# Kernel optimization log

Measured on AMD Instinct MI355X. Metric: run time of the kernel, lower is better.

The kernel has to match this reference:

```python
import jax, jax.numpy as jnp
import numpy as np

EMBED_DIM = 128


def setup_inputs() -> dict:
    key = jax.random.key(0)
    k = jax.random.split(key, 6)
    B, S, H, D = 4, 512, 768, EMBED_DIM
    ent_embeddings = jax.random.normal(k[0], (B, S, H), jnp.float32)
    ent_type_ids = jax.random.randint(k[1], (B, S), 0, 10)  # entity-type labels (>=0)
    ent_mask = jax.random.randint(k[2], (B, S), 0, 2)       # 0/1 attention mask
    W_mu = jax.random.normal(k[3], (H, D), jnp.float32) / np.sqrt(H)
    b_mu = jnp.zeros((D,), jnp.float32)
    W_sigma = jax.random.normal(k[4], (H, D), jnp.float32) / np.sqrt(H)
    b_sigma = jnp.zeros((D,), jnp.float32)
    return dict(ent_embeddings=ent_embeddings, ent_type_ids=ent_type_ids, ent_mask=ent_mask,
                W_mu=W_mu, b_mu=b_mu, W_sigma=W_sigma, b_sigma=b_sigma)


def _pairwise_kl(mu, sigma, dim):
    # Symmetrized KL between diagonal Gaussians for all pairs (i=row, j=col).
    # Decomposed into rank-D contractions instead of materializing [N,N,D].
    inv = 1.0 / sigma                               # [N,D]
    S_log = jnp.sum(jnp.log(sigma), axis=1)         # [N] sum_d log sigma (1e-14 inside log is negligible in fp32)
    A = jnp.einsum('id,jd->ij', inv, sigma)         # sum_d sigma_j/sigma_i
    q = jnp.sum(mu * mu * inv, axis=1)              # [N] sum_d mu_i^2/sigma_i
    cross = jnp.einsum('id,jd->ij', mu * inv, mu)   # sum_d mu_i*mu_j/sigma_i
    quad = jnp.einsum('id,jd->ij', inv, mu * mu)    # sum_d mu_j^2/sigma_i
    md_i = q[:, None] - 2.0 * cross + quad          # sum_d (mu_i-mu_j)^2 / sigma_i
    ld = S_log[None, :] - S_log[:, None]            # sum_d log(sigma_j/sigma_i)
    ij_kl = 0.5 * (A + md_i - dim - ld)
    ji_kl = 0.5 * (A.T + md_i.T - dim + ld)
    return 0.5 * (ij_kl + ji_kl)


def reference(ent_embeddings, ent_type_ids, ent_mask, W_mu, b_mu, W_sigma, b_sigma):
    D = EMBED_DIM
    h = jax.nn.relu(ent_embeddings)                 # dropout in eval mode (identity)
    mu = (h @ W_mu + b_mu).reshape(-1, D)           # [N,D]
    sigma = (jax.nn.elu(h @ W_sigma + b_sigma) + 1.0 + 1e-14).reshape(-1, D)

    labels = ent_type_ids.reshape(-1)
    valid = (ent_mask.reshape(-1) == 1) & (labels >= 0)   # consider_mutual_O=True: no labels>0 filter

    # loss_mask: ALL coordinates of mu differ (kills diagonal / duplicate rows)
    alldiff = jnp.all(mu[:, None, :] != mu[None, :, :], axis=-1)  # [N,N]
    pair_valid = valid[:, None] & valid[None, :]
    lab_eq = labels[:, None] == labels[None, :]
    denom_m = (alldiff & pair_valid).astype(mu.dtype)             # loss_mask
    num_w = (lab_eq & alldiff & pair_valid).astype(mu.dtype)      # loss_weights

    loss = -_pairwise_kl(mu, sigma, D)              # loss_type='KL'

    # NT-Xent, temperature=1
    e = jnp.exp(loss)
    cnts = jnp.sum(num_w, axis=1)
    loss_num = jnp.sum(e * num_w, axis=1)
    loss_den = jnp.sum(e * denom_m, axis=1)
    sel = cnts > 0
    safe = lambda v: jnp.where(sel, v, 1.0)
    lf = -jnp.log2(safe(loss_num)) + jnp.log2(safe(loss_den)) + jnp.log2(safe(cnts))
    n_sel = jnp.maximum(jnp.sum(sel.astype(mu.dtype)), 1.0)
    return jnp.sum(jnp.where(sel, lf, 0.0)) / n_sel
```

## Files before the change

kernel.cpp:

```cpp
#include <hip/hip_runtime.h>
#include <math.h>

#define NROWS 2048
#define HDIM 768
#define DDIM 128
#define FEAT 512
#define DCAP 2048
#define TSLOTS 8192

typedef __attribute__((ext_vector_type(8))) short bf16x8;
typedef __attribute__((ext_vector_type(4))) float f32x4;

__device__ __forceinline__ void mergeState(float& m, float& n, float& d,
                                           float m2, float n2, float d2) {
  float M = fmaxf(m, m2);
  float s1 = (m >= M) ? 1.0f : __expf(m - M);
  float s2 = (m2 >= M) ? 1.0f : __expf(m2 - M);
  n = n * s1 + n2 * s2;
  d = d * s1 + d2 * s2;
  m = M;
}

__device__ __forceinline__ unsigned short bfhi(float x) {
  unsigned int u = __float_as_uint(x);
  return (unsigned short)((u + 0x7fffu + ((u >> 16) & 1u)) >> 16);
}

__global__ __launch_bounds__(256) void k1m(
    const float* __restrict__ E, const float* __restrict__ Wmu,
    const float* __restrict__ Wsg, float* __restrict__ Cpart,
    unsigned long long* __restrict__ tab, int* __restrict__ rowflag,
    int* __restrict__ dupcnt, float* __restrict__ gsum)
{
  __shared__ unsigned short lds[12288];
  const int t = threadIdx.x;
  const int bid = blockIdx.x;

  if (t < 32) tab[bid * 32 + t] = 0ULL;
  if (t < 8)  rowflag[bid * 8 + t] = 0;
  if (bid == 0 && t == 0) {
    dupcnt[0] = 0;
    gsum[0] = 0.f; gsum[1] = 0.f; gsum[2] = 0.f;
  }

  const int mt = bid & 31, nt = (bid >> 5) & 1, ks = bid >> 6;
  const int i0 = mt * 64, kbase = ks * 192;
  const float* Wsrc = nt ? Wsg : Wmu;

  const int akg = t & 3, arow = t >> 2;
  const int bcol = t & 127, bkh = t >> 7;
  const int aw  = akg * 512 + arow * 8;
  const int bw0 = 2048 + (bkh * 2) * 1024 + bcol * 8;
  const int bw1 = bw0 + 1024;

  float4 rA0, rA1; float rB[16];

  auto loadRegs = [&](int it) {
    const int ka = kbase + it * 32;
    const float* ep = E + (size_t)(i0 + arow) * HDIM + ka + akg * 8;
    rA0 = *reinterpret_cast<const float4*>(ep);
    rA1 = *reinterpret_cast<const float4*>(ep + 4);
    const float* wp = Wsrc + (size_t)(ka + bkh * 16) * DDIM + bcol;
    #pragma unroll
    for (int j = 0; j < 16; ++j) rB[j] = wp[(size_t)j * DDIM];
  };

  auto writeLds = [&](int buf) {
    unsigned short* lb = lds + buf * 6144;
    unsigned short ha[8];
    ha[0] = bfhi(fmaxf(rA0.x, 0.f)); ha[1] = bfhi(fmaxf(rA0.y, 0.f));
    ha[2] = bfhi(fmaxf(rA0.z, 0.f)); ha[3] = bfhi(fmaxf(rA0.w, 0.f));
    ha[4] = bfhi(fmaxf(rA1.x, 0.f)); ha[5] = bfhi(fmaxf(rA1.y, 0.f));
    ha[6] = bfhi(fmaxf(rA1.z, 0.f)); ha[7] = bfhi(fmaxf(rA1.w, 0.f));
    *reinterpret_cast<ushort4*>(lb + aw)     = make_ushort4(ha[0], ha[1], ha[2], ha[3]);
    *reinterpret_cast<ushort4*>(lb + aw + 4) = make_ushort4(ha[4], ha[5], ha[6], ha[7]);
    unsigned short hb[16];
    #pragma unroll
    for (int j = 0; j < 16; ++j) hb[j] = bfhi(rB[j]);
    *reinterpret_cast<ushort4*>(lb + bw0)     = make_ushort4(hb[0],  hb[1],  hb[2],  hb[3]);
    *reinterpret_cast<ushort4*>(lb + bw0 + 4) = make_ushort4(hb[4],  hb[5],  hb[6],  hb[7]);
    *reinterpret_cast<ushort4*>(lb + bw1)     = make_ushort4(hb[8],  hb[9],  hb[10], hb[11]);
    *reinterpret_cast<ushort4*>(lb + bw1 + 4) = make_ushort4(hb[12], hb[13], hb[14], hb[15]);
  };

  f32x4 acc[2][4];
  #pragma unroll
  for (int a = 0; a < 2; ++a)
    #pragma unroll
    for (int b = 0; b < 4; ++b) {
      acc[a][b][0] = 0.f; acc[a][b][1] = 0.f; acc[a][b][2] = 0.f; acc[a][b][3] = 0.f;
    }

  const int wid = t >> 6, lane = t & 63;
  const int wr = wid >> 1, wc = wid & 1;
  const int gq = lane >> 4, c0 = lane & 15;

  loadRegs(0);
  writeLds(0);
  loadRegs(1);
  __syncthreads();

  for (int it = 0; it < 6; ++it) {
    {
      const unsigned short* lb = lds + (it & 1) * 6144;
      bf16x8 ah[2], bh[4];
      #pragma unroll
      for (int fa = 0; fa < 2; ++fa) {
        const int ia = gq * 512 + (wr * 32 + fa * 16 + c0) * 8;
        ah[fa] = *reinterpret_cast<const bf16x8*>(lb + ia);
      }
      #pragma unroll
      for (int fb = 0; fb < 4; ++fb) {
        const int ib = 2048 + gq * 1024 + (wc * 64 + fb * 16 + c0) * 8;
        bh[fb] = *reinterpret_cast<const bf16x8*>(lb + ib);
      }
      #pragma unroll
      for (int fa = 0; fa < 2; ++fa)
        #pragma unroll
        for (int fb = 0; fb < 4; ++fb)
          acc[fa][fb] = __builtin_amdgcn_mfma_f32_16x16x32_bf16(
              ah[fa], bh[fb], acc[fa][fb], 0, 0, 0);
    }
    if (it < 5) {
      writeLds((it + 1) & 1);
      if (it < 4) loadRegs(it + 2);
    }
    __syncthreads();
  }

  const int n0 = nt * 128;
  #pragma unroll
  for (int fa = 0; fa < 2; ++fa)
    #pragma unroll
    for (int fb = 0; fb < 4; ++fb)
      #pragma unroll
      for (int r = 0; r < 4; ++r) {
        const int row = i0 + wr * 32 + fa * 16 + gq * 4 + r;
        const int col = n0 + wc * 64 + fb * 16 + c0;
        Cpart[((size_t)ks * NROWS + row) * 256 + col] = acc[fa][fb][r];
      }
}

__global__ __launch_bounds__(256) void k1e(
    const float* __restrict__ Cpart, const float* __restrict__ bmu,
    const float* __restrict__ bsg,
    unsigned short* __restrict__ Ftl,
    float* __restrict__ qout, unsigned long long* __restrict__ tab,
    int* __restrict__ rowflag, int* __restrict__ dupcnt,
    int2* __restrict__ duplist)
{
  __shared__ unsigned short fbuf[16][520];
  const int t = threadIdx.x;
  const int row16 = t >> 4, cw = t & 15, c8 = cw * 8;
  const int g = blockIdx.x;
  const int rg = g * 16 + row16;

  float vm[8], vs[8];
  #pragma unroll
  for (int j = 0; j < 8; ++j) { vm[j] = 0.f; vs[j] = 0.f; }
  #pragma unroll
  for (int ks = 0; ks < 4; ++ks) {
    const float* src = &Cpart[((size_t)ks * NROWS + rg) * 256];
    float4 m0 = *reinterpret_cast<const float4*>(src + c8);
    float4 m1 = *reinterpret_cast<const float4*>(src + c8 + 4);
    float4 s0 = *reinterpret_cast<const float4*>(src + 128 + c8);
    float4 s1 = *reinterpret_cast<const float4*>(src + 128 + c8 + 4);
    vm[0] += m0.x; vm[1] += m0.y; vm[2] += m0.z; vm[3] += m0.w;
    vm[4] += m1.x; vm[5] += m1.y; vm[6] += m1.z; vm[7] += m1.w;
    vs[0] += s0.x; vs[1] += s0.y; vs[2] += s0.z; vs[3] += s0.w;
    vs[4] += s1.x; vs[5] += s1.y; vs[6] += s1.z; vs[7] += s1.w;
  }

  float q = 0.f;
  unsigned int hx = 0u, hs2 = 0u;
  unsigned short o1[8], o2[8], o3[8], o4[8];
  #pragma unroll
  for (int j = 0; j < 8; ++j) {
    const int col = c8 + j;
    float z = vs[j] + bsg[col];
    float s = (z > 0.f ? z + 1.0f : __expf(z)) + 1e-14f;
    float mu = vm[j] + bmu[col];
    float inv = 1.0f / s;
    o1[j] = bfhi(inv);
    o2[j] = bfhi(s + mu * mu);
    o3[j] = bfhi(-2.0f * mu * inv);
    o4[j] = bfhi(mu);
    q += mu * mu * inv;
    unsigned int b = __float_as_uint(mu);
    if (b == 0x80000000u) b = 0u;
    unsigned int hm = (b ^ ((unsigned int)col * 0x9E3779B9u)) * 0x85EBCA6Bu;
    hm ^= hm >> 13;
    hx ^= hm;
    hs2 += hm * 0xC2B2AE35u;
  }
  *reinterpret_cast<ushort4*>(&fbuf[row16][      c8])     = make_ushort4(o1[0], o1[1], o1[2], o1[3]);
  *reinterpret_cast<ushort4*>(&fbuf[row16][      c8 + 4]) = make_ushort4(o1[4], o1[5], o1[6], o1[7]);
  *reinterpret_cast<ushort4*>(&fbuf[row16][128 + c8])     = make_ushort4(o2[0], o2[1], o2[2], o2[3]);
  *reinterpret_cast<ushort4*>(&fbuf[row16][128 + c8 + 4]) = make_ushort4(o2[4], o2[5], o2[6], o2[7]);
  *reinterpret_cast<ushort4*>(&fbuf[row16][256 + c8])     = make_ushort4(o3[0], o3[1], o3[2], o3[3]);
  *reinterpret_cast<ushort4*>(&fbuf[row16][256 + c8 + 4]) = make_ushort4(o3[4], o3[5], o3[6], o3[7]);
  *reinterpret_cast<ushort4*>(&fbuf[row16][384 + c8])     = make_ushort4(o4[0], o4[1], o4[2], o4[3]);
  *reinterpret_cast<ushort4*>(&fbuf[row16][384 + c8 + 4]) = make_ushort4(o4[4], o4[5], o4[6], o4[7]);

  #pragma unroll
  for (int o = 8; o; o >>= 1) q += __shfl_xor(q, o, 16);
  #pragma unroll
  for (int o = 1; o < 16; o <<= 1) {
    hx  ^= (unsigned int)__shfl_xor((int)hx, o, 16);
    hs2 += (unsigned int)__shfl_xor((int)hs2, o, 16);
  }
  if (cw == 0) {
    qout[rg] = q;
    unsigned long long key = (((unsigned long long)hx << 32) | hs2) & ~0xFFFULL;
    if (key == 0ULL) key = 0x123456789000ULL;
    const unsigned long long me = key | (unsigned long long)(rg + 1);
    unsigned int h = (hx ^ (hs2 * 0x9E3779B9u)) & (TSLOTS - 1);
    for (;;) {
      unsigned long long old = atomicCAS(&tab[h], 0ULL, me);
      if (old == 0ULL) break;
      if ((old & ~0xFFFULL) == key) {
        int r2 = (int)(old & 0xFFFULL) - 1;
        rowflag[rg] = 1; rowflag[r2] = 1;
        int e = atomicAdd(dupcnt, 1);
        if (e < DCAP) duplist[e] = make_int2(min(rg, r2), max(rg, r2));
      }
      h = (h + 1u) & (TSLOTS - 1);
    }
  }
  __syncthreads();

  #pragma unroll
  for (int u = 0; u < 4; ++u) {
    const int f = u * 256 + t;
    const int kb = f >> 6, ln = f & 63;
    const int gq2 = ln >> 4, cc = ln & 15;
    uint4 v = *reinterpret_cast<const uint4*>(&fbuf[cc][kb * 32 + gq2 * 8]);
    *reinterpret_cast<uint4*>(&Ftl[((size_t)(g * 16 + kb)) * 512 + ln * 8]) = v;
  }
}

__global__ __launch_bounds__(1024, 4) void k2_mfma(
    const unsigned short* __restrict__ Ftl,
    const float* __restrict__ qv, const int* __restrict__ labels,
    const int* __restrict__ msk, const int* __restrict__ rowflag,
    const int* __restrict__ dupcnt, const int2* __restrict__ duplist,
    float4* __restrict__ ipart)
{
  __shared__ unsigned short Blds[65536];
  const int t = threadIdx.x;
  const int orig = blockIdx.x;
  const int xcd = orig & 7, idx = orig >> 3;
  const int bi = (xcd >> 1) * 4 + (idx >> 3);
  const int bj = (xcd & 1) * 8 + (idx & 7);
  const int i0 = bi * 128, j0 = bj * 128;
  const int wid = t >> 6, lane = t & 63;
  const int wr = wid >> 2, wc = wid & 3;
  const int gq = lane >> 4, c0 = lane & 15;

  {
    const unsigned short* Bsrc = Ftl + (size_t)bj * 65536;
    #pragma unroll
    for (int u = 0; u < 8; ++u) {
      const int slot = u * 1024 + t;
      uint4 v = *reinterpret_cast<const uint4*>(Bsrc + slot * 8);
      *reinterpret_cast<uint4*>(Blds + slot * 8) = v;
    }
  }
  __syncthreads();

  const int ga0 = bi * 8 + wr * 2;
  const unsigned short* fl = Ftl + lane * 8;
  const unsigned short* bl = Blds + lane * 8;
  const int hb0 = wc * 2;

  f32x4 acc[2][2];
  #pragma unroll
  for (int a = 0; a < 2; ++a)
    #pragma unroll
    for (int b = 0; b < 2; ++b) {
      acc[a][b][0] = 0.f; acc[a][b][1] = 0.f; acc[a][b][2] = 0.f; acc[a][b][3] = 0.f;
    }

  bf16x8 Abuf[3][2];

#define LOADA(kb_, s_)                                                         \
  {                                                                            \
    Abuf[s_][0] = *reinterpret_cast<const bf16x8*>(fl + ((ga0    ) * 16 + (kb_)) * 512); \
    Abuf[s_][1] = *reinterpret_cast<const bf16x8*>(fl + ((ga0 + 1) * 16 + (kb_)) * 512); \
  }

#define STEP(kb_, s_)                                                          \
  {                                                                            \
    const int kbb_ = (kb_) ^ 4;                                                \
    bf16x8 B0 = *reinterpret_cast<const bf16x8*>(bl + ((hb0    ) * 16 + kbb_) * 512); \
    bf16x8 B1 = *reinterpret_cast<const bf16x8*>(bl + ((hb0 + 1) * 16 + kbb_) * 512); \
    acc[0][0] = __builtin_amdgcn_mfma_f32_16x16x32_bf16(Abuf[s_][0], B0, acc[0][0], 0, 0, 0); \
    acc[0][1] = __builtin_amdgcn_mfma_f32_16x16x32_bf16(Abuf[s_][0], B1, acc[0][1], 0, 0, 0); \
    acc[1][0] = __builtin_amdgcn_mfma_f32_16x16x32_bf16(Abuf[s_][1], B0, acc[1][0], 0, 0, 0); \
    acc[1][1] = __builtin_amdgcn_mfma_f32_16x16x32_bf16(Abuf[s_][1], B1, acc[1][1], 0, 0, 0); \
  }

  LOADA(0, 0);
  LOADA(1, 1);
  #pragma unroll
  for (int kb = 0; kb < 16; ++kb) {
    if (kb < 14) { LOADA(kb + 2, (kb + 2) % 3); }
    STEP(kb, kb % 3);
  }
#undef LOADA
#undef STEP

  const int ndup = min(dupcnt[0], DCAP);
  int ljv[2]; float qjv[2]; int fjv[2]; int gjv[2];
  #pragma unroll
  for (int fb = 0; fb < 2; ++fb) {
    const int gj = j0 + wc * 32 + fb * 16 + c0;
    const int lab = labels[gj];
    ljv[fb] = (msk[gj] == 1 && lab >= 0) ? lab : -1;
    qjv[fb] = qv[gj];
    fjv[fb] = rowflag[gj];
    gjv[fb] = gj;
  }
  #pragma unroll
  for (int fa = 0; fa < 2; ++fa) {
    const int ibase = i0 + wr * 32 + fa * 16 + gq * 4;
    int li4[4], mi4[4], fi4[4]; float qi4[4];
    *reinterpret_cast<int4*>(li4)   = *reinterpret_cast<const int4*>(labels + ibase);
    *reinterpret_cast<int4*>(mi4)   = *reinterpret_cast<const int4*>(msk + ibase);
    *reinterpret_cast<int4*>(fi4)   = *reinterpret_cast<const int4*>(rowflag + ibase);
    *reinterpret_cast<float4*>(qi4) = *reinterpret_cast<const float4*>(qv + ibase);
    #pragma unroll
    for (int r = 0; r < 4; ++r) {
      const int gi = ibase + r;
      const int li = (mi4[r] == 1 && li4[r] >= 0) ? li4[r] : -1;
      float m = -INFINITY, n = 0.f, d = 0.f, c = 0.f;
      if (li >= 0) {
        #pragma unroll
        for (int fb = 0; fb < 2; ++fb) {
          const int lj = ljv[fb];
          bool inc = (lj >= 0) && (gi != gjv[fb]);
          if (inc && fi4[r] && fjv[fb]) {
            int plo = min(gi, gjv[fb]), phi = max(gi, gjv[fb]);
            for (int e = 0; e < ndup; ++e) {
              int2 p = duplist[e];
              if (p.x == plo && p.y == phi) { inc = false; break; }
            }
          }
          if (inc) {
            float S = acc[fa][fb][r];
            float l = 64.0f - 0.25f * (qi4[r] + qjv[fb] + S);
            float w = (li == lj) ? 1.0f : 0.0f;
            mergeState(m, n, d, l, w, 1.0f);
            c += w;
          }
        }
      }
      #pragma unroll
      for (int o = 1; o < 16; o <<= 1) {
        float m2 = __shfl_xor(m, o);
        float n2 = __shfl_xor(n, o);
        float d2 = __shfl_xor(d, o);
        float c2 = __shfl_xor(c, o);
        mergeState(m, n, d, m2, n2, d2);
        c += c2;
      }
      if (c0 == 0)
        ipart[(size_t)(bj * 4 + wc) * NROWS + gi] = make_float4(m, n, d, c);
    }
  }
}

__global__ __launch_bounds__(256) void k3(const float4* __restrict__ ipart,
                                          float* __restrict__ gsum,
                                          float* __restrict__ out)
{
  const int r = blockIdx.x * 256 + threadIdx.x;
  float m = -INFINITY, n = 0.f, d = 0.f, c = 0.f;
  #pragma unroll 8
  for (int js = 0; js < 64; ++js) {
    float4 p = ipart[(size_t)js * NROWS + r];
    mergeState(m, n, d, p.x, p.y, p.z);
    c += p.w;
  }
  float lf = 0.f, ns = 0.f;
  if (c > 0.f) {
    lf = log2f(d) - log2f(n) + log2f(c);
    ns = 1.f;
  }
  #pragma unroll
  for (int o = 32; o; o >>= 1) {
    lf += __shfl_down(lf, o);
    ns += __shfl_down(ns, o);
  }
  __shared__ float sl[4], sn[4];
  const int wid = threadIdx.x >> 6;
  if ((threadIdx.x & 63) == 0) { sl[wid] = lf; sn[wid] = ns; }
  __syncthreads();
  if (threadIdx.x == 0) {
    float L = sl[0] + sl[1] + sl[2] + sl[3];
    float C = sn[0] + sn[1] + sn[2] + sn[3];
    atomicAdd(&gsum[0], L);
    atomicAdd(&gsum[1], C);
    __threadfence();
    unsigned int tk = atomicAdd(reinterpret_cast<unsigned int*>(gsum + 2), 1u);
    if (tk == 7u) {
      float Lt = atomicAdd(&gsum[0], 0.f);
      float Ct = atomicAdd(&gsum[1], 0.f);
      out[0] = Lt / fmaxf(Ct, 1.0f);
    }
  }
}

extern "C" void kernel_launch(void* const* d_in, const int* in_sizes, int n_in,
                              void* d_out, int out_size, void* d_ws, size_t ws_size,
                              hipStream_t stream) {
  const float* E   = (const float*)d_in[0];
  const int*   tid = (const int*)d_in[1];
  const int*   msk = (const int*)d_in[2];
  const float* Wmu = (const float*)d_in[3];
  const float* bmu = (const float*)d_in[4];
  const float* Wsg = (const float*)d_in[5];
  const float* bsg = (const float*)d_in[6];

  unsigned char* w = (unsigned char*)d_ws;
  unsigned short* Ftl  = (unsigned short*)w;  w += (size_t)NROWS * FEAT * 2;
  float* Cpart         = (float*)w;           w += (size_t)4 * NROWS * 256 * 4;
  float* qv            = (float*)w;           w += (size_t)NROWS * 4;
  unsigned long long* tab = (unsigned long long*)w; w += (size_t)TSLOTS * 8;
  int* rowflag         = (int*)w;             w += (size_t)NROWS * 4;
  int* dupcnt          = (int*)w;             w += 256;
  float* gsum          = (float*)w;           w += 256;
  int2* duplist        = (int2*)w;            w += (size_t)DCAP * 8;
  float4* ipart        = (float4*)w;          w += (size_t)64 * NROWS * 16;

  k1m<<<256, 256, 0, stream>>>(E, Wmu, Wsg, Cpart, tab, rowflag, dupcnt, gsum);
  k1e<<<128, 256, 0, stream>>>(Cpart, bmu, bsg, Ftl, qv,
                               tab, rowflag, dupcnt, duplist);
  k2_mfma<<<256, 1024, 0, stream>>>(Ftl, qv, tid, msk, rowflag,
                                    dupcnt, duplist, ipart);
  k3<<<8, 256, 0, stream>>>(ipart, gsum, (float*)d_out);
}
```

Baseline: 45.25 us.

## Fuse final reduction into MFMA kernel via last-block ticket; deepen A prefetch

Removes the separate k3 launch. Each k2 block takes an atomic ticket, and the last of the 256 blocks merges all ipart partial states for every row and writes the final loss. The A-operand register prefetch also deepens from 3 to 4 stages, with the first loads issued before the B tile is staged into LDS to overlap global latency. In exchange, the final reduction now runs serially in a single block after all others finish, and the extra prefetch stage adds register pressure.

Result: slower. 67.56 us (+49.3%).

```diff
diff --git a/kernel.cpp b/kernel.cpp
--- a/kernel.cpp
+++ b/kernel.cpp
@@ -244,7 +244,8 @@
     const float* __restrict__ qv, const int* __restrict__ labels,
     const int* __restrict__ msk, const int* __restrict__ rowflag,
     const int* __restrict__ dupcnt, const int2* __restrict__ duplist,
-    float4* __restrict__ ipart)
+    float4* __restrict__ ipart, float* __restrict__ gsum,
+    float* __restrict__ out)
 {
   __shared__ unsigned short Blds[65536];
   const int t = threadIdx.x;
@@ -257,6 +258,23 @@
   const int wr = wid >> 2, wc = wid & 3;
   const int gq = lane >> 4, c0 = lane & 15;
 
+  const int ga0 = bi * 8 + wr * 2;
+  const unsigned short* fl = Ftl + lane * 8;
+  const unsigned short* bl = Blds + lane * 8;
+  const int hb0 = wc * 2;
+
+  bf16x8 Abuf[4][2];
+
+#define LOADA(kb_, s_)                                                         \
+  {                                                                            \
+    Abuf[s_][0] = *reinterpret_cast<const bf16x8*>(fl + ((ga0    ) * 16 + (kb_)) * 512); \
+    Abuf[s_][1] = *reinterpret_cast<const bf16x8*>(fl + ((ga0 + 1) * 16 + (kb_)) * 512); \
+  }
+
+  LOADA(0, 0);
+  LOADA(1, 1);
+  LOADA(2, 2);
+
   {
     const unsigned short* Bsrc = Ftl + (size_t)bj * 65536;
     #pragma unroll
@@ -268,11 +286,6 @@
   }
   __syncthreads();
 
-  const int ga0 = bi * 8 + wr * 2;
-  const unsigned short* fl = Ftl + lane * 8;
-  const unsigned short* bl = Blds + lane * 8;
-  const int hb0 = wc * 2;
-
   f32x4 acc[2][2];
   #pragma unroll
   for (int a = 0; a < 2; ++a)
@@ -280,14 +293,6 @@
     for (int b = 0; b < 2; ++b) {
       acc[a][b][0] = 0.f; acc[a][b][1] = 0.f; acc[a][b][2] = 0.f; acc[a][b][3] = 0.f;
     }
-
-  bf16x8 Abuf[3][2];
-
-#define LOADA(kb_, s_)                                                         \
-  {                                                                            \
-    Abuf[s_][0] = *reinterpret_cast<const bf16x8*>(fl + ((ga0    ) * 16 + (kb_)) * 512); \
-    Abuf[s_][1] = *reinterpret_cast<const bf16x8*>(fl + ((ga0 + 1) * 16 + (kb_)) * 512); \
-  }
 
 #define STEP(kb_, s_)                                                          \
   {                                                                            \
@@ -300,12 +305,10 @@
     acc[1][1] = __builtin_amdgcn_mfma_f32_16x16x32_bf16(Abuf[s_][1], B1, acc[1][1], 0, 0, 0); \
   }
 
-  LOADA(0, 0);
-  LOADA(1, 1);
   #pragma unroll
   for (int kb = 0; kb < 16; ++kb) {
-    if (kb < 14) { LOADA(kb + 2, (kb + 2) % 3); }
-    STEP(kb, kb % 3);
+    if (kb < 13) { LOADA(kb + 3, (kb + 3) & 3); }
+    STEP(kb, kb & 3);
   }
 #undef LOADA
 #undef STEP
@@ -368,45 +371,44 @@
         ipart[(size_t)(bj * 4 + wc) * NROWS + gi] = make_float4(m, n, d, c);
     }
   }
-}
-
-__global__ __launch_bounds__(256) void k3(const float4* __restrict__ ipart,
-                                          float* __restrict__ gsum,
-                                          float* __restrict__ out)
-{
-  const int r = blockIdx.x * 256 + threadIdx.x;
-  float m = -INFINITY, n = 0.f, d = 0.f, c = 0.f;
-  #pragma unroll 8
-  for (int js = 0; js < 64; ++js) {
-    float4 p = ipart[(size_t)js * NROWS + r];
-    mergeState(m, n, d, p.x, p.y, p.z);
-    c += p.w;
-  }
-  float lf = 0.f, ns = 0.f;
-  if (c > 0.f) {
-    lf = log2f(d) - log2f(n) + log2f(c);
-    ns = 1.f;
-  }
-  #pragma unroll
-  for (int o = 32; o; o >>= 1) {
-    lf += __shfl_down(lf, o);
-    ns += __shfl_down(ns, o);
-  }
-  __shared__ float sl[4], sn[4];
-  const int wid = threadIdx.x >> 6;
-  if ((threadIdx.x & 63) == 0) { sl[wid] = lf; sn[wid] = ns; }
+
   __syncthreads();
-  if (threadIdx.x == 0) {
-    float L = sl[0] + sl[1] + sl[2] + sl[3];
-    float C = sn[0] + sn[1] + sn[2] + sn[3];
-    atomicAdd(&gsum[0], L);
-    atomicAdd(&gsum[1], C);
+  __shared__ unsigned int tkS;
+  if (t == 0) {
     __threadfence();
-    unsigned int tk = atomicAdd(reinterpret_cast<unsigned int*>(gsum + 2), 1u);
-    if (tk == 7u) {
-      float Lt = atomicAdd(&gsum[0], 0.f);
-      float Ct = atomicAdd(&gsum[1], 0.f);
-      out[0] = Lt / fmaxf(Ct, 1.0f);
+    tkS = atomicAdd(reinterpret_cast<unsigned int*>(gsum + 2), 1u);
+  }
+  __syncthreads();
+  if (tkS == 255u) {
+    __threadfence();
+    float lfsum = 0.f, nssum = 0.f;
+    #pragma unroll
+    for (int rr = 0; rr < 2; ++rr) {
+      const int r = rr * 1024 + t;
+      float m = -INFINITY, n = 0.f, d = 0.f, c = 0.f;
+      for (int js = 0; js < 64; ++js) {
+        float4 p = ipart[(size_t)js * NROWS + r];
+        mergeState(m, n, d, p.x, p.y, p.z);
+        c += p.w;
+      }
+      if (c > 0.f) {
+        lfsum += log2f(d) - log2f(n) + log2f(c);
+        nssum += 1.f;
+      }
+    }
+    #pragma unroll
+    for (int o = 32; o; o >>= 1) {
+      lfsum += __shfl_down(lfsum, o);
+      nssum += __shfl_down(nssum, o);
+    }
+    float* fl2 = reinterpret_cast<float*>(Blds);
+    if (lane == 0) { fl2[wid] = lfsum; fl2[16 + wid] = nssum; }
+    __syncthreads();
+    if (t == 0) {
+      float L = 0.f, C = 0.f;
+      #pragma unroll
+      for (int u = 0; u < 16; ++u) { L += fl2[u]; C += fl2[16 + u]; }
+      out[0] = L / fmaxf(C, 1.0f);
     }
   }
 }
@@ -437,6 +439,6 @@
   k1e<<<128, 256, 0, stream>>>(Cpart, bmu, bsg, Ftl, qv,
                                tab, rowflag, dupcnt, duplist);
   k2_mfma<<<256, 1024, 0, stream>>>(Ftl, qv, tid, msk, rowflag,
-                                    dupcnt, duplist, ipart);
-  k3<<<8, 256, 0, stream>>>(ipart, gsum, (float*)d_out);
-}
+                                    dupcnt, duplist, ipart, gsum,
+                                    (float*)d_out);
+}
```
